# Optimization experiments

Measured on AMD Instinct MI355X. Metric: run time of the kernel, lower is better.

## Reference

```python
import jax, jax.numpy as jnp
import numpy as np

HIDDEN = 1024
N_HEADS = 16
HEAD_DIM = HIDDEN // N_HEADS


def setup_inputs() -> dict:
    key = jax.random.key(0)
    ks = jax.random.split(key, 10)
    s = 0.02
    return {
        "x": jax.random.normal(ks[0], (2, 2048, HIDDEN), dtype=jnp.float32),
        "wq_w": jax.random.normal(ks[1], (HEAD_DIM, HEAD_DIM), dtype=jnp.float32) * s,
        "wq_b": jax.random.normal(ks[2], (HEAD_DIM,), dtype=jnp.float32) * s,
        "wk_w": jax.random.normal(ks[3], (HEAD_DIM, HEAD_DIM), dtype=jnp.float32) * s,
        "wk_b": jax.random.normal(ks[4], (HEAD_DIM,), dtype=jnp.float32) * s,
        "wv_w": jax.random.normal(ks[5], (HEAD_DIM, HEAD_DIM), dtype=jnp.float32) * s,
        "wv_b": jax.random.normal(ks[6], (HEAD_DIM,), dtype=jnp.float32) * s,
        "wo_w": jax.random.normal(ks[7], (HIDDEN, HIDDEN), dtype=jnp.float32) * s,
        "wo_b": jax.random.normal(ks[8], (HIDDEN,), dtype=jnp.float32) * s,
    }


def reference(x, wq_w, wq_b, wk_w, wk_b, wv_w, wv_b, wo_w, wo_b):
    B, S, _ = x.shape
    # Faithful to torch: plain reshape (view), NOT a transpose-based head split.
    xh = x.reshape(B, N_HEADS, S, HEAD_DIM)  # [B,H,S,D]
    # torch Linear: y = x @ W.T + b
    Q = jnp.einsum('bhsd,ed->bhse', xh, wq_w) + wq_b
    K = jnp.einsum('bhsd,ed->bhse', xh, wk_w) + wk_b
    V = jnp.einsum('bhsd,ed->bhse', xh, wv_w) + wv_b
    scale = 1.0 / jnp.sqrt(jnp.float32(HEAD_DIM))
    scores = jnp.einsum('bhqd,bhkd->bhqk', Q, K) * scale  # [B,H,S,S]
    attn = jax.nn.softmax(scores, axis=-1)
    ctx = jnp.einsum('bhqk,bhkd->bhqd', attn, V)  # [B,H,S,D]
    out = ctx.reshape(B, S, HIDDEN)
    return out @ wo_w.T + wo_b
```

## Files before the change

### kernel.cpp

```cpp
#include <hip/hip_runtime.h>
#include <hip/hip_bf16.h>

#define SEQ 2048
#define BHCOUNT 32
#define NROWS (BHCOUNT*SEQ)

typedef unsigned short u16;
typedef unsigned int u32;
using bf16x8 = __attribute__((ext_vector_type(8))) short;
using f32x4  = __attribute__((ext_vector_type(4))) float;

__device__ __forceinline__ float bf2f(u16 h) {
    return __uint_as_float(((u32)h) << 16);
}
__device__ __forceinline__ u16 f2bf(float f) {
    u32 u = __float_as_uint(f);
    u32 r = (u + 0x7FFFu + ((u >> 16) & 1u)) >> 16;
    return (u16)r;
}
__device__ __forceinline__ float fexp2(float x) {
    float r; asm("v_exp_f32 %0, %1" : "=v"(r) : "v"(x)); return r;
}

__device__ __forceinline__ void gload16(const u16* g, u16* l) {
    __builtin_amdgcn_global_load_lds(
        (const __attribute__((address_space(1))) u32*)g,
        (__attribute__((address_space(3))) u32*)l, 16, 0, 0);
}

__device__ __forceinline__ void cvt8(const float* src, float sc, u16* o) {
    float4 a = *(const float4*)src;
    float4 b = *(const float4*)(src + 4);
    o[0]=f2bf(a.x*sc); o[1]=f2bf(a.y*sc); o[2]=f2bf(a.z*sc); o[3]=f2bf(a.w*sc);
    o[4]=f2bf(b.x*sc); o[5]=f2bf(b.y*sc); o[6]=f2bf(b.z*sc); o[7]=f2bf(b.w*sc);
}

__global__ __launch_bounds__(256) void qkv_wconv_kernel(
    const float* __restrict__ x,
    const float* __restrict__ wq, const float* __restrict__ bq,
    const float* __restrict__ wk, const float* __restrict__ bk,
    const float* __restrict__ wv, const float* __restrict__ bv,
    const float* __restrict__ wo,
    u16* __restrict__ Q, u16* __restrict__ K, u16* __restrict__ Vg,
    u16* __restrict__ wob_t)
{
    __shared__ u16 xs[128*64];
    __shared__ u16 ws[192*64];
    __shared__ float bs[192];
    const int t = threadIdx.x;

    if (blockIdx.x >= 512) {
        int g = (blockIdx.x - 512)*256 + t;
        int tile = g >> 9, within = g & 511;
        int row = within >> 3, ks = within & 7;
        int cb = tile >> 4, kt = tile & 15;
        u16 o[8];
        cvt8(&wo[(size_t)(cb*64 + row)*1024 + kt*64 + ks*8], 1.f, o);
        *(uint4*)&wob_t[(size_t)g*8] = *(uint4*)o;
        return;
    }

    const int wid = t >> 6, lane = t & 63;
    const int ln = lane & 15, g4 = lane >> 4;
    const int blk = blockIdx.x;
    const int m0 = blk * 128;
    const int bh = blk >> 4;
    const int ktg0 = (blk & 15) * 2;
    const float qscale = 0.125f * 1.44269504f;

    #pragma unroll
    for (int c = 0; c < 6; ++c) {
        int slot = c*256 + t;
        int row = slot >> 3, ks = slot & 7;
        const float* wsrc = (c < 2) ? wq : (c < 4) ? wk : wv;
        float sc = (c < 2) ? qscale : 1.f;
        u16 o[8];
        cvt8(&wsrc[(row & 63)*64 + ks*8], sc, o);
        *(uint4*)&ws[row*64 + ((ks ^ (row & 7)) << 3)] = *(uint4*)o;
    }
    #pragma unroll
    for (int c = 0; c < 4; ++c) {
        int slot = c*256 + t;
        int row = slot >> 3, ks = slot & 7;
        u16 o[8];
        cvt8(&x[(size_t)(m0 + row)*64 + ks*8], 1.f, o);
        *(uint4*)&xs[row*64 + ((ks ^ (row & 7)) << 3)] = *(uint4*)o;
    }
    if (t < 192) {
        int p = t >> 6, e = t & 63;
        bs[t] = (p == 0) ? bq[e]*qscale : (p == 1) ? bk[e] : bv[e];
    }
    __syncthreads();

    bf16x8 af[2][2];
    #pragma unroll
    for (int mf = 0; mf < 2; ++mf)
        #pragma unroll
        for (int kf = 0; kf < 2; ++kf) {
            int arow = wid*32 + mf*16 + ln;
            af[mf][kf] = *(const bf16x8*)&xs[arow*64 + (((kf*4 + g4) ^ (arow & 7)) << 3)];
        }

    #pragma unroll
    for (int p = 0; p < 2; ++p) {
        bf16x8 bfr[4][2];
        #pragma unroll
        for (int nt = 0; nt < 4; ++nt)
            #pragma unroll
            for (int kf = 0; kf < 2; ++kf) {
                int brow = p*64 + nt*16 + ln;
                bfr[nt][kf] = *(const bf16x8*)&ws[brow*64 + (((kf*4 + g4) ^ (ln & 7)) << 3)];
            }
        f32x4 acc[2][4];
        #pragma unroll
        for (int mf = 0; mf < 2; ++mf)
            #pragma unroll
            for (int nt = 0; nt < 4; ++nt) acc[mf][nt] = (f32x4){0.f,0.f,0.f,0.f};
        #pragma unroll
        for (int kf = 0; kf < 2; ++kf)
            #pragma unroll
            for (int mf = 0; mf < 2; ++mf)
                #pragma unroll
                for (int nt = 0; nt < 4; ++nt)
                    acc[mf][nt] = __builtin_amdgcn_mfma_f32_16x16x32_bf16(
                        af[mf][kf], bfr[nt][kf], acc[mf][nt], 0, 0, 0);
        u16* dst = p ? K : Q;
        #pragma unroll
        for (int mf = 0; mf < 2; ++mf)
            #pragma unroll
            for (int nt = 0; nt < 4; ++nt) {
                float bv4 = bs[p*64 + nt*16 + ln];
                #pragma unroll
                for (int r = 0; r < 4; ++r)
                    dst[(size_t)(m0 + wid*32 + mf*16 + g4*4 + r)*64 + nt*16 + ln]
                        = f2bf(acc[mf][nt][r] + bv4);
            }
    }

    bf16x8 wvf[4][2];
    #pragma unroll
    for (int et = 0; et < 4; ++et)
        #pragma unroll
        for (int kf = 0; kf < 2; ++kf) {
            int brow = 128 + et*16 + ln;
            wvf[et][kf] = *(const bf16x8*)&ws[brow*64 + (((kf*4 + g4) ^ (ln & 7)) << 3)];
        }
    f32x4 vacc[4][2];
    #pragma unroll
    for (int et = 0; et < 4; ++et)
        #pragma unroll
        for (int st = 0; st < 2; ++st) vacc[et][st] = (f32x4){0.f,0.f,0.f,0.f};
    #pragma unroll
    for (int kf = 0; kf < 2; ++kf)
        #pragma unroll
        for (int et = 0; et < 4; ++et)
            #pragma unroll
            for (int st = 0; st < 2; ++st)
                vacc[et][st] = __builtin_amdgcn_mfma_f32_16x16x32_bf16(
                    wvf[et][kf], af[st][kf], vacc[et][st], 0, 0, 0);

    __syncthreads();
    u16* vstage = xs;
    #pragma unroll
    for (int et = 0; et < 4; ++et)
        #pragma unroll
        for (int st = 0; st < 2; ++st)
            #pragma unroll
            for (int r = 0; r < 4; ++r) {
                int e = et*16 + g4*4 + r;
                int s = wid*32 + st*16 + ln;
                vstage[e*128 + ((s + 2*e) & 127)] = f2bf(vacc[et][st][r] + bs[128 + e]);
            }
    __syncthreads();

    #pragma unroll
    for (int c = 0; c < 8; ++c) {
        int j = c*256 + t;
        int kt2 = j >> 10, within = j & 1023;
        int ee = within >> 4, kp0 = (within & 15) * 4;
        int sbase = ((kp0 & 4) << 3) | ((kp0 & 32) >> 1) | ((kp0 & 24) >> 1);
        u16 o[4];
        #pragma unroll
        for (int i = 0; i < 4; ++i)
            o[i] = vstage[ee*128 + ((kt2*64 + sbase + i + 2*ee) & 127)];
        *(uint2*)&Vg[((size_t)bh*32 + ktg0 + kt2)*4096 + ee*64 + kp0] = *(uint2*)o;
    }
}

__device__ __forceinline__ void qkt_tile(
    const u16* Ks, const int (&foff)[4][2], const bf16x8 (&qf)[2], f32x4 (&sacc)[4])
{
    __builtin_amdgcn_s_setprio(1);
    #pragma unroll
    for (int nt = 0; nt < 4; ++nt) {
        sacc[nt] = (f32x4){0.f, 0.f, 0.f, 0.f};
        #pragma unroll
        for (int kf = 0; kf < 2; ++kf)
            sacc[nt] = __builtin_amdgcn_mfma_f32_16x16x32_bf16(
                *(const bf16x8*)&Ks[foff[nt][kf]], qf[kf], sacc[nt], 0, 0, 0);
    }
    __builtin_amdgcn_s_setprio(0);
}

__device__ __forceinline__ void sm_pv(
    f32x4 (&sacc)[4], f32x4 (&oacc)[4], f32x4& lacc,
    const u16* Vts, const int (&foff)[4][2], const bf16x8& ones)
{
    #pragma unroll
    for (int nt = 0; nt < 4; ++nt)
        #pragma unroll
        for (int r = 0; r < 4; ++r)
            sacc[nt][r] = fexp2(sacc[nt][r]);

    union PU { u32 w[4]; bf16x8 v; } pu0, pu1;
    asm("v_cvt_pk_bf16_f32 %0, %1, %2" : "=v"(pu0.w[0]) : "v"(sacc[0][0]), "v"(sacc[0][1]));
    asm("v_cvt_pk_bf16_f32 %0, %1, %2" : "=v"(pu0.w[1]) : "v"(sacc[0][2]), "v"(sacc[0][3]));
    asm("v_cvt_pk_bf16_f32 %0, %1, %2" : "=v"(pu0.w[2]) : "v"(sacc[2][0]), "v"(sacc[2][1]));
    asm("v_cvt_pk_bf16_f32 %0, %1, %2" : "=v"(pu0.w[3]) : "v"(sacc[2][2]), "v"(sacc[2][3]));
    asm("v_cvt_pk_bf16_f32 %0, %1, %2" : "=v"(pu1.w[0]) : "v"(sacc[1][0]), "v"(sacc[1][1]));
    asm("v_cvt_pk_bf16_f32 %0, %1, %2" : "=v"(pu1.w[1]) : "v"(sacc[1][2]), "v"(sacc[1][3]));
    asm("v_cvt_pk_bf16_f32 %0, %1, %2" : "=v"(pu1.w[2]) : "v"(sacc[3][0]), "v"(sacc[3][1]));
    asm("v_cvt_pk_bf16_f32 %0, %1, %2" : "=v"(pu1.w[3]) : "v"(sacc[3][2]), "v"(sacc[3][3]));
    bf16x8 pf[2] = { pu0.v, pu1.v };

    __builtin_amdgcn_s_setprio(1);
    #pragma unroll
    for (int dt = 0; dt < 4; ++dt)
        #pragma unroll
        for (int kf = 0; kf < 2; ++kf)
            oacc[dt] = __builtin_amdgcn_mfma_f32_16x16x32_bf16(
                pf[kf], *(const bf16x8*)&Vts[foff[dt][kf]], oacc[dt], 0, 0, 0);
    #pragma unroll
    for (int kf = 0; kf < 2; ++kf)
        lacc = __builtin_amdgcn_mfma_f32_16x16x32_bf16(pf[kf], ones, lacc, 0, 0, 0);
    __builtin_amdgcn_s_setprio(0);
}

__global__ __launch_bounds__(512) void attn_kernel(
    const u16* __restrict__ Q, const u16* __restrict__ K,
    const u16* __restrict__ Vg, u16* __restrict__ ctx)
{
    __shared__ u16 Kls[3*4096];
    __shared__ u16 Vls[3*4096];

    const int t = threadIdx.x;
    const int wid = t >> 6, lane = t & 63;
    const int ln = lane & 15, g4 = lane >> 4;
    const int bh = blockIdx.y;
    const size_t base   = (size_t)bh * SEQ * 64;
    const size_t vgbase = (size_t)bh * 32 * 4096;
    const int q0 = blockIdx.x * 128 + wid * 16;

    int goff;
    {
        int row = t >> 3, ks = t & 7;
        goff = row*64 + ((ks ^ (row & 7)) << 3);
    }
    const int ldst = wid * 512;

    int foff[4][2];
    #pragma unroll
    for (int nt = 0; nt < 4; ++nt)
        #pragma unroll
        for (int kf = 0; kf < 2; ++kf) {
            int frow = nt*16 + ln;
            foff[nt][kf] = frow*64 + (((kf*4 + g4) ^ (frow & 7)) << 3);
        }

    bf16x8 qf[2];
    #pragma unroll
    for (int kf = 0; kf < 2; ++kf)
        qf[kf] = *(const bf16x8*)&Q[base + (size_t)(q0 + ln)*64 + kf*32 + g4*8];

    bf16x8 ones;
    #pragma unroll
    for (int i = 0; i < 8; ++i) ones[i] = (short)0x3F80;

    f32x4 oacc[4];
    #pragma unroll
    for (int i = 0; i < 4; ++i) oacc[i] = (f32x4){0.f, 0.f, 0.f, 0.f};
    f32x4 lacc = (f32x4){0.f, 0.f, 0.f, 0.f};

    gload16(&K [base   + goff], &Kls[ldst]);
    gload16(&Vg[vgbase + goff], &Vls[ldst]);
    gload16(&K [base   + 4096 + goff], &Kls[4096 + ldst]);
    gload16(&Vg[vgbase + 4096 + goff], &Vls[4096 + ldst]);
    const u16* kptr = &K [base   + 2*4096 + goff];
    const u16* vptr = &Vg[vgbase + 2*4096 + goff];
    __syncthreads();

    f32x4 sA[4], sB[4];
    qkt_tile(&Kls[0], foff, qf, sA);

    #define ABODY(PREV, CUR, SP, SC, SN, STG)                               \
        do {                                                                \
            __syncthreads();                                                \
            if (STG) {                                                      \
                gload16(kptr, &Kls[(SN)*4096 + ldst]);                      \
                gload16(vptr, &Vls[(SN)*4096 + ldst]);                      \
                kptr += 4096; vptr += 4096;                                 \
            }                                                               \
            qkt_tile(&Kls[(SC)*4096], foff, qf, CUR);                       \
            sm_pv(PREV, oacc, lacc, &Vls[(SP)*4096], foff, ones);           \
        } while (0)

    for (int c = 0; c < 5; ++c) {
        ABODY(sA, sB, 0, 1, 2, 1);
        ABODY(sB, sA, 1, 2, 0, 1);
        ABODY(sA, sB, 2, 0, 1, 1);
        ABODY(sB, sA, 0, 1, 2, 1);
        ABODY(sA, sB, 1, 2, 0, 1);
        ABODY(sB, sA, 2, 0, 1, 1);
    }
    ABODY(sA, sB, 0, 1, 2, 0);
    sm_pv(sB, oacc, lacc, &Vls[1*4096], foff, ones);

    #undef ABODY

    #pragma unroll
    for (int r = 0; r < 4; ++r) {
        float inv = 1.f / lacc[r];
        size_t row = base + (size_t)(q0 + g4*4 + r)*64;
        #pragma unroll
        for (int dt = 0; dt < 4; ++dt)
            ctx[row + dt*16 + ln] = f2bf(oacc[dt][r] * inv);
    }
}

__global__ __launch_bounds__(256) void oproj_kernel(
    const u16* __restrict__ ctx, const u16* __restrict__ wob_t,
    const float* __restrict__ bo, float* __restrict__ out)
{
    __shared__ u16 Als[2][128*64];
    __shared__ u16 Bls[2][64*64];
    const int t = threadIdx.x;
    const int wid = t >> 6, lane = t & 63;
    const int ln = lane & 15, g4 = lane >> 4;
    const int wr = wid >> 1, wc = wid & 1;
    const int rb = blockIdx.x, cb = blockIdx.y;
    const int m0 = rb * 128;

    int gA[4], gB[2];
    #pragma unroll
    for (int c = 0; c < 4; ++c) {
        int slot = c*256 + t;
        int row = slot >> 3, ks = slot & 7;
        gA[c] = row*1024 + ((ks ^ (row & 7)) << 3);
    }
    #pragma unroll
    for (int c = 0; c < 2; ++c) {
        int slot = c*256 + t;
        int row = slot >> 3, ks = slot & 7;
        gB[c] = row*64 + ((ks ^ (row & 7)) << 3);
    }
    const u16* actx = ctx + (size_t)m0*1024;
    const u16* bw   = wob_t + (size_t)cb*16*4096;

    f32x4 acc[4][2];
    #pragma unroll
    for (int mf = 0; mf < 4; ++mf)
        #pragma unroll
        for (int nf = 0; nf < 2; ++nf)
            acc[mf][nf] = (f32x4){0.f, 0.f, 0.f, 0.f};

    #pragma unroll
    for (int c = 0; c < 4; ++c) gload16(&actx[gA[c]], &Als[0][(c*256+t)*8]);
    #pragma unroll
    for (int c = 0; c < 2; ++c) gload16(&bw[gB[c]],   &Bls[0][(c*256+t)*8]);
    __syncthreads();

    for (int kt2 = 0; kt2 < 8; ++kt2) {
        #pragma unroll
        for (int half = 0; half < 2; ++half) {
            const int kt = kt2*2 + half;
            if (kt < 15) {
                #pragma unroll
                for (int c = 0; c < 4; ++c)
                    gload16(&actx[(kt+1)*64 + gA[c]], &Als[half^1][(c*256+t)*8]);
                #pragma unroll
                for (int c = 0; c < 2; ++c)
                    gload16(&bw[(kt+1)*4096 + gB[c]], &Bls[half^1][(c*256+t)*8]);
            }
            const u16* As = Als[half];
            const u16* Bs = Bls[half];

            __builtin_amdgcn_s_setprio(1);
            #pragma unroll
            for (int kf = 0; kf < 2; ++kf) {
                bf16x8 af[4], bfr[2];
                #pragma unroll
                for (int mf = 0; mf < 4; ++mf) {
                    int arow = wr*64 + mf*16 + ln;
                    af[mf] = *(const bf16x8*)&As[arow*64 + (((kf*4 + g4) ^ (arow & 7)) << 3)];
                }
                #pragma unroll
                for (int nf = 0; nf < 2; ++nf) {
                    int brow = wc*32 + nf*16 + ln;
                    bfr[nf] = *(const bf16x8*)&Bs[brow*64 + (((kf*4 + g4) ^ (brow & 7)) << 3)];
                }
                #pragma unroll
                for (int mf = 0; mf < 4; ++mf)
                    #pragma unroll
                    for (int nf = 0; nf < 2; ++nf)
                        acc[mf][nf] = __builtin_amdgcn_mfma_f32_16x16x32_bf16(
                            af[mf], bfr[nf], acc[mf][nf], 0, 0, 0);
            }
            __builtin_amdgcn_s_setprio(0);

            __syncthreads();
        }
    }

    #pragma unroll
    for (int mf = 0; mf < 4; ++mf)
        #pragma unroll
        for (int r = 0; r < 4; ++r) {
            int m = m0 + wr*64 + mf*16 + g4*4 + r;
            #pragma unroll
            for (int nf = 0; nf < 2; ++nf) {
                int col = cb*64 + wc*32 + nf*16 + ln;
                out[(size_t)m*1024 + col] = acc[mf][nf][r] + bo[col];
            }
        }
}

extern "C" void kernel_launch(void* const* d_in, const int* in_sizes, int n_in,
                              void* d_out, int out_size, void* d_ws, size_t ws_size,
                              hipStream_t stream) {
    (void)in_sizes; (void)n_in; (void)out_size; (void)ws_size;
    const float* x  = (const float*)d_in[0];
    const float* wq = (const float*)d_in[1];
    const float* bq = (const float*)d_in[2];
    const float* wk = (const float*)d_in[3];
    const float* bk = (const float*)d_in[4];
    const float* wv = (const float*)d_in[5];
    const float* bv = (const float*)d_in[6];
    const float* wo = (const float*)d_in[7];
    const float* bo = (const float*)d_in[8];
    float* out = (float*)d_out;

    u16* Qb  = (u16*)d_ws;
    u16* Kb  = Qb + (size_t)NROWS*64;
    u16* Vgb = Kb + (size_t)NROWS*64;
    u16* ctx = Vgb + (size_t)NROWS*64;
    u16* wob_t = ctx + (size_t)NROWS*64;

    qkv_wconv_kernel<<<dim3(1024), 256, 0, stream>>>(
        x, wq, bq, wk, bk, wv, bv, wo, Qb, Kb, Vgb, wob_t);
    attn_kernel<<<dim3(16, 32), 512, 0, stream>>>(Qb, Kb, Vgb, ctx);
    oproj_kernel<<<dim3(32, 16), 256, 0, stream>>>(ctx, wob_t, bo, out);
}
```

Before: 71.40 us.

## Give each attention wave two query tiles, reusing K/V fragments with double buffering

The attention kernel now launches 256-thread blocks where each wave handles 32 query rows (two 16-row tiles). Each K and V fragment read from LDS feeds two MFMAs, which halves LDS fragment traffic per unit of work. The old triple-buffered, software-pipelined loop that overlapped QK^T of one tile with softmax·V of the previous one is replaced by a simpler double-buffered loop with one barrier per tile. The trade-offs are fewer waves per block, higher register pressure, and the loss of the cross-tile overlap between QK^T and PV.

```diff
diff --git a/kernel.cpp b/kernel.cpp
--- a/kernel.cpp
+++ b/kernel.cpp
@@ -187,61 +187,12 @@
     }
 }
 
-__device__ __forceinline__ void qkt_tile(
-    const u16* Ks, const int (&foff)[4][2], const bf16x8 (&qf)[2], f32x4 (&sacc)[4])
-{
-    __builtin_amdgcn_s_setprio(1);
-    #pragma unroll
-    for (int nt = 0; nt < 4; ++nt) {
-        sacc[nt] = (f32x4){0.f, 0.f, 0.f, 0.f};
-        #pragma unroll
-        for (int kf = 0; kf < 2; ++kf)
-            sacc[nt] = __builtin_amdgcn_mfma_f32_16x16x32_bf16(
-                *(const bf16x8*)&Ks[foff[nt][kf]], qf[kf], sacc[nt], 0, 0, 0);
-    }
-    __builtin_amdgcn_s_setprio(0);
-}
-
-__device__ __forceinline__ void sm_pv(
-    f32x4 (&sacc)[4], f32x4 (&oacc)[4], f32x4& lacc,
-    const u16* Vts, const int (&foff)[4][2], const bf16x8& ones)
-{
-    #pragma unroll
-    for (int nt = 0; nt < 4; ++nt)
-        #pragma unroll
-        for (int r = 0; r < 4; ++r)
-            sacc[nt][r] = fexp2(sacc[nt][r]);
-
-    union PU { u32 w[4]; bf16x8 v; } pu0, pu1;
-    asm("v_cvt_pk_bf16_f32 %0, %1, %2" : "=v"(pu0.w[0]) : "v"(sacc[0][0]), "v"(sacc[0][1]));
-    asm("v_cvt_pk_bf16_f32 %0, %1, %2" : "=v"(pu0.w[1]) : "v"(sacc[0][2]), "v"(sacc[0][3]));
-    asm("v_cvt_pk_bf16_f32 %0, %1, %2" : "=v"(pu0.w[2]) : "v"(sacc[2][0]), "v"(sacc[2][1]));
-    asm("v_cvt_pk_bf16_f32 %0, %1, %2" : "=v"(pu0.w[3]) : "v"(sacc[2][2]), "v"(sacc[2][3]));
-    asm("v_cvt_pk_bf16_f32 %0, %1, %2" : "=v"(pu1.w[0]) : "v"(sacc[1][0]), "v"(sacc[1][1]));
-    asm("v_cvt_pk_bf16_f32 %0, %1, %2" : "=v"(pu1.w[1]) : "v"(sacc[1][2]), "v"(sacc[1][3]));
-    asm("v_cvt_pk_bf16_f32 %0, %1, %2" : "=v"(pu1.w[2]) : "v"(sacc[3][0]), "v"(sacc[3][1]));
-    asm("v_cvt_pk_bf16_f32 %0, %1, %2" : "=v"(pu1.w[3]) : "v"(sacc[3][2]), "v"(sacc[3][3]));
-    bf16x8 pf[2] = { pu0.v, pu1.v };
-
-    __builtin_amdgcn_s_setprio(1);
-    #pragma unroll
-    for (int dt = 0; dt < 4; ++dt)
-        #pragma unroll
-        for (int kf = 0; kf < 2; ++kf)
-            oacc[dt] = __builtin_amdgcn_mfma_f32_16x16x32_bf16(
-                pf[kf], *(const bf16x8*)&Vts[foff[dt][kf]], oacc[dt], 0, 0, 0);
-    #pragma unroll
-    for (int kf = 0; kf < 2; ++kf)
-        lacc = __builtin_amdgcn_mfma_f32_16x16x32_bf16(pf[kf], ones, lacc, 0, 0, 0);
-    __builtin_amdgcn_s_setprio(0);
-}
-
-__global__ __launch_bounds__(512) void attn_kernel(
+__global__ __launch_bounds__(256, 2) void attn_kernel(
     const u16* __restrict__ Q, const u16* __restrict__ K,
     const u16* __restrict__ Vg, u16* __restrict__ ctx)
 {
-    __shared__ u16 Kls[3*4096];
-    __shared__ u16 Vls[3*4096];
+    __shared__ u16 Kls[2][4096];
+    __shared__ u16 Vls[2][4096];
 
     const int t = threadIdx.x;
     const int wid = t >> 6, lane = t & 63;
@@ -249,14 +200,15 @@
     const int bh = blockIdx.y;
     const size_t base   = (size_t)bh * SEQ * 64;
     const size_t vgbase = (size_t)bh * 32 * 4096;
-    const int q0 = blockIdx.x * 128 + wid * 16;
-
-    int goff;
-    {
-        int row = t >> 3, ks = t & 7;
-        goff = row*64 + ((ks ^ (row & 7)) << 3);
-    }
-    const int ldst = wid * 512;
+    const int q0 = blockIdx.x * 128 + wid * 32;
+
+    int goff[2];
+    #pragma unroll
+    for (int c = 0; c < 2; ++c) {
+        int s = c*256 + t;
+        int row = s >> 3, ks = s & 7;
+        goff[c] = row*64 + ((ks ^ (row & 7)) << 3);
+    }
 
     int foff[4][2];
     #pragma unroll
@@ -267,63 +219,125 @@
             foff[nt][kf] = frow*64 + (((kf*4 + g4) ^ (frow & 7)) << 3);
         }
 
-    bf16x8 qf[2];
-    #pragma unroll
-    for (int kf = 0; kf < 2; ++kf)
-        qf[kf] = *(const bf16x8*)&Q[base + (size_t)(q0 + ln)*64 + kf*32 + g4*8];
+    bf16x8 qf0[2], qf1[2];
+    #pragma unroll
+    for (int kf = 0; kf < 2; ++kf) {
+        qf0[kf] = *(const bf16x8*)&Q[base + (size_t)(q0 + ln)*64      + kf*32 + g4*8];
+        qf1[kf] = *(const bf16x8*)&Q[base + (size_t)(q0 + 16 + ln)*64 + kf*32 + g4*8];
+    }
 
     bf16x8 ones;
     #pragma unroll
     for (int i = 0; i < 8; ++i) ones[i] = (short)0x3F80;
 
-    f32x4 oacc[4];
-    #pragma unroll
-    for (int i = 0; i < 4; ++i) oacc[i] = (f32x4){0.f, 0.f, 0.f, 0.f};
-    f32x4 lacc = (f32x4){0.f, 0.f, 0.f, 0.f};
-
-    gload16(&K [base   + goff], &Kls[ldst]);
-    gload16(&Vg[vgbase + goff], &Vls[ldst]);
-    gload16(&K [base   + 4096 + goff], &Kls[4096 + ldst]);
-    gload16(&Vg[vgbase + 4096 + goff], &Vls[4096 + ldst]);
-    const u16* kptr = &K [base   + 2*4096 + goff];
-    const u16* vptr = &Vg[vgbase + 2*4096 + goff];
+    f32x4 oacc0[4], oacc1[4];
+    #pragma unroll
+    for (int i = 0; i < 4; ++i) {
+        oacc0[i] = (f32x4){0.f, 0.f, 0.f, 0.f};
+        oacc1[i] = (f32x4){0.f, 0.f, 0.f, 0.f};
+    }
+    f32x4 lacc0 = (f32x4){0.f, 0.f, 0.f, 0.f};
+    f32x4 lacc1 = (f32x4){0.f, 0.f, 0.f, 0.f};
+
+    #pragma unroll
+    for (int c = 0; c < 2; ++c) {
+        gload16(&K [base   + goff[c]], &Kls[0][c*2048 + wid*512]);
+        gload16(&Vg[vgbase + goff[c]], &Vls[0][c*2048 + wid*512]);
+    }
     __syncthreads();
 
-    f32x4 sA[4], sB[4];
-    qkt_tile(&Kls[0], foff, qf, sA);
-
-    #define ABODY(PREV, CUR, SP, SC, SN, STG)                               \
-        do {                                                                \
-            __syncthreads();                                                \
-            if (STG) {                                                      \
-                gload16(kptr, &Kls[(SN)*4096 + ldst]);                      \
-                gload16(vptr, &Vls[(SN)*4096 + ldst]);                      \
-                kptr += 4096; vptr += 4096;                                 \
-            }                                                               \
-            qkt_tile(&Kls[(SC)*4096], foff, qf, CUR);                       \
-            sm_pv(PREV, oacc, lacc, &Vls[(SP)*4096], foff, ones);           \
-        } while (0)
-
-    for (int c = 0; c < 5; ++c) {
-        ABODY(sA, sB, 0, 1, 2, 1);
-        ABODY(sB, sA, 1, 2, 0, 1);
-        ABODY(sA, sB, 2, 0, 1, 1);
-        ABODY(sB, sA, 0, 1, 2, 1);
-        ABODY(sA, sB, 1, 2, 0, 1);
-        ABODY(sB, sA, 2, 0, 1, 1);
-    }
-    ABODY(sA, sB, 0, 1, 2, 0);
-    sm_pv(sB, oacc, lacc, &Vls[1*4096], foff, ones);
-
-    #undef ABODY
+    for (int kt2 = 0; kt2 < 16; ++kt2) {
+        #pragma unroll
+        for (int half = 0; half < 2; ++half) {
+            const int kt = kt2*2 + half;
+            if (kt < 31) {
+                #pragma unroll
+                for (int c = 0; c < 2; ++c) {
+                    gload16(&K [base   + (size_t)(kt+1)*4096 + goff[c]],
+                            &Kls[half^1][c*2048 + wid*512]);
+                    gload16(&Vg[vgbase + (size_t)(kt+1)*4096 + goff[c]],
+                            &Vls[half^1][c*2048 + wid*512]);
+                }
+            }
+            const u16* Ks  = Kls[half];
+            const u16* Vts = Vls[half];
+
+            f32x4 s0[4], s1[4];
+            #pragma unroll
+            for (int nt = 0; nt < 4; ++nt) {
+                s0[nt] = (f32x4){0.f, 0.f, 0.f, 0.f};
+                s1[nt] = (f32x4){0.f, 0.f, 0.f, 0.f};
+            }
+            __builtin_amdgcn_s_setprio(1);
+            #pragma unroll
+            for (int nt = 0; nt < 4; ++nt)
+                #pragma unroll
+                for (int kf = 0; kf < 2; ++kf) {
+                    bf16x8 kfr = *(const bf16x8*)&Ks[foff[nt][kf]];
+                    s0[nt] = __builtin_amdgcn_mfma_f32_16x16x32_bf16(kfr, qf0[kf], s0[nt], 0, 0, 0);
+                    s1[nt] = __builtin_amdgcn_mfma_f32_16x16x32_bf16(kfr, qf1[kf], s1[nt], 0, 0, 0);
+                }
+            __builtin_amdgcn_s_setprio(0);
+
+            #pragma unroll
+            for (int nt = 0; nt < 4; ++nt)
+                #pragma unroll
+                for (int r = 0; r < 4; ++r) {
+                    s0[nt][r] = fexp2(s0[nt][r]);
+                    s1[nt][r] = fexp2(s1[nt][r]);
+                }
+
+            union PU { u32 w[4]; bf16x8 v; } a0, a1, b0, b1;
+            asm("v_cvt_pk_bf16_f32 %0, %1, %2" : "=v"(a0.w[0]) : "v"(s0[0][0]), "v"(s0[0][1]));
+            asm("v_cvt_pk_bf16_f32 %0, %1, %2" : "=v"(a0.w[1]) : "v"(s0[0][2]), "v"(s0[0][3]));
+            asm("v_cvt_pk_bf16_f32 %0, %1, %2" : "=v"(a0.w[2]) : "v"(s0[2][0]), "v"(s0[2][1]));
+            asm("v_cvt_pk_bf16_f32 %0, %1, %2" : "=v"(a0.w[3]) : "v"(s0[2][2]), "v"(s0[2][3]));
+            asm("v_cvt_pk_bf16_f32 %0, %1, %2" : "=v"(a1.w[0]) : "v"(s0[1][0]), "v"(s0[1][1]));
+            asm("v_cvt_pk_bf16_f32 %0, %1, %2" : "=v"(a1.w[1]) : "v"(s0[1][2]), "v"(s0[1][3]));
+            asm("v_cvt_pk_bf16_f32 %0, %1, %2" : "=v"(a1.w[2]) : "v"(s0[3][0]), "v"(s0[3][1]));
+            asm("v_cvt_pk_bf16_f32 %0, %1, %2" : "=v"(a1.w[3]) : "v"(s0[3][2]), "v"(s0[3][3]));
+            asm("v_cvt_pk_bf16_f32 %0, %1, %2" : "=v"(b0.w[0]) : "v"(s1[0][0]), "v"(s1[0][1]));
+            asm("v_cvt_pk_bf16_f32 %0, %1, %2" : "=v"(b0.w[1]) : "v"(s1[0][2]), "v"(s1[0][3]));
+            asm("v_cvt_pk_bf16_f32 %0, %1, %2" : "=v"(b0.w[2]) : "v"(s1[2][0]), "v"(s1[2][1]));
+            asm("v_cvt_pk_bf16_f32 %0, %1, %2" : "=v"(b0.w[3]) : "v"(s1[2][2]), "v"(s1[2][3]));
+            asm("v_cvt_pk_bf16_f32 %0, %1, %2" : "=v"(b1.w[0]) : "v"(s1[1][0]), "v"(s1[1][1]));
+            asm("v_cvt_pk_bf16_f32 %0, %1, %2" : "=v"(b1.w[1]) : "v"(s1[1][2]), "v"(s1[1][3]));
+            asm("v_cvt_pk_bf16_f32 %0, %1, %2" : "=v"(b1.w[2]) : "v"(s1[3][0]), "v"(s1[3][1]));
+            asm("v_cvt_pk_bf16_f32 %0, %1, %2" : "=v"(b1.w[3]) : "v"(s1[3][2]), "v"(s1[3][3]));
+            bf16x8 pf0[2] = { a0.v, a1.v };
+            bf16x8 pf1[2] = { b0.v, b1.v };
+
+            __builtin_amdgcn_s_setprio(1);
+            #pragma unroll
+            for (int dt = 0; dt < 4; ++dt)
+                #pragma unroll
+                for (int kf = 0; kf < 2; ++kf) {
+                    bf16x8 vfr = *(const bf16x8*)&Vts[foff[dt][kf]];
+                    oacc0[dt] = __builtin_amdgcn_mfma_f32_16x16x32_bf16(pf0[kf], vfr, oacc0[dt], 0, 0, 0);
+                    oacc1[dt] = __builtin_amdgcn_mfma_f32_16x16x32_bf16(pf1[kf], vfr, oacc1[dt], 0, 0, 0);
+                }
+            #pragma unroll
+            for (int kf = 0; kf < 2; ++kf) {
+                lacc0 = __builtin_amdgcn_mfma_f32_16x16x32_bf16(pf0[kf], ones, lacc0, 0, 0, 0);
+                lacc1 = __builtin_amdgcn_mfma_f32_16x16x32_bf16(pf1[kf], ones, lacc1, 0, 0, 0);
+            }
+            __builtin_amdgcn_s_setprio(0);
+
+            __syncthreads();
+        }
+    }
 
     #pragma unroll
     for (int r = 0; r < 4; ++r) {
-        float inv = 1.f / lacc[r];
-        size_t row = base + (size_t)(q0 + g4*4 + r)*64;
-        #pragma unroll
-        for (int dt = 0; dt < 4; ++dt)
-            ctx[row + dt*16 + ln] = f2bf(oacc[dt][r] * inv);
+        float inv0 = 1.f / lacc0[r];
+        float inv1 = 1.f / lacc1[r];
+        size_t row0 = base + (size_t)(q0 + g4*4 + r)*64;
+        size_t row1 = base + (size_t)(q0 + 16 + g4*4 + r)*64;
+        #pragma unroll
+        for (int dt = 0; dt < 4; ++dt) {
+            ctx[row0 + dt*16 + ln] = f2bf(oacc0[dt][r] * inv0);
+            ctx[row1 + dt*16 + ln] = f2bf(oacc1[dt][r] * inv1);
+        }
     }
 }
 
@@ -447,6 +461,6 @@
 
     qkv_wconv_kernel<<<dim3(1024), 256, 0, stream>>>(
         x, wq, bq, wk, bk, wv, bv, wo, Qb, Kb, Vgb, wob_t);
-    attn_kernel<<<dim3(16, 32), 512, 0, stream>>>(Qb, Kb, Vgb, ctx);
+    attn_kernel<<<dim3(16, 32), 256, 0, stream>>>(Qb, Kb, Vgb, ctx);
     oproj_kernel<<<dim3(32, 16), 256, 0, stream>>>(ctx, wob_t, bo, out);
 }
```

Result: no change. 70.76 us (-0.9%).

## Shrink attention blocks to four waves with a simple double-buffered K/V loop

Applied to the files above, without the earlier changes.

The attention kernel moves from 512-thread blocks covering 128 queries to 256-thread blocks covering 64 queries, which doubles the grid and allows up to four blocks per CU. The triple-buffered K/V ring is replaced by a double buffer. The QK^T of the next tile no longer overlaps the softmax/PV of the previous one; each tile now runs QK^T, exp and PV back to back, followed by a barrier. The aim is better latency hiding through occupancy and finer load balancing, at the cost of reading K/V from global memory twice as often and losing the explicit software pipelining.

```diff
diff --git a/kernel.cpp b/kernel.cpp
--- a/kernel.cpp
+++ b/kernel.cpp
@@ -187,61 +187,12 @@
     }
 }
 
-__device__ __forceinline__ void qkt_tile(
-    const u16* Ks, const int (&foff)[4][2], const bf16x8 (&qf)[2], f32x4 (&sacc)[4])
-{
-    __builtin_amdgcn_s_setprio(1);
-    #pragma unroll
-    for (int nt = 0; nt < 4; ++nt) {
-        sacc[nt] = (f32x4){0.f, 0.f, 0.f, 0.f};
-        #pragma unroll
-        for (int kf = 0; kf < 2; ++kf)
-            sacc[nt] = __builtin_amdgcn_mfma_f32_16x16x32_bf16(
-                *(const bf16x8*)&Ks[foff[nt][kf]], qf[kf], sacc[nt], 0, 0, 0);
-    }
-    __builtin_amdgcn_s_setprio(0);
-}
-
-__device__ __forceinline__ void sm_pv(
-    f32x4 (&sacc)[4], f32x4 (&oacc)[4], f32x4& lacc,
-    const u16* Vts, const int (&foff)[4][2], const bf16x8& ones)
-{
-    #pragma unroll
-    for (int nt = 0; nt < 4; ++nt)
-        #pragma unroll
-        for (int r = 0; r < 4; ++r)
-            sacc[nt][r] = fexp2(sacc[nt][r]);
-
-    union PU { u32 w[4]; bf16x8 v; } pu0, pu1;
-    asm("v_cvt_pk_bf16_f32 %0, %1, %2" : "=v"(pu0.w[0]) : "v"(sacc[0][0]), "v"(sacc[0][1]));
-    asm("v_cvt_pk_bf16_f32 %0, %1, %2" : "=v"(pu0.w[1]) : "v"(sacc[0][2]), "v"(sacc[0][3]));
-    asm("v_cvt_pk_bf16_f32 %0, %1, %2" : "=v"(pu0.w[2]) : "v"(sacc[2][0]), "v"(sacc[2][1]));
-    asm("v_cvt_pk_bf16_f32 %0, %1, %2" : "=v"(pu0.w[3]) : "v"(sacc[2][2]), "v"(sacc[2][3]));
-    asm("v_cvt_pk_bf16_f32 %0, %1, %2" : "=v"(pu1.w[0]) : "v"(sacc[1][0]), "v"(sacc[1][1]));
-    asm("v_cvt_pk_bf16_f32 %0, %1, %2" : "=v"(pu1.w[1]) : "v"(sacc[1][2]), "v"(sacc[1][3]));
-    asm("v_cvt_pk_bf16_f32 %0, %1, %2" : "=v"(pu1.w[2]) : "v"(sacc[3][0]), "v"(sacc[3][1]));
-    asm("v_cvt_pk_bf16_f32 %0, %1, %2" : "=v"(pu1.w[3]) : "v"(sacc[3][2]), "v"(sacc[3][3]));
-    bf16x8 pf[2] = { pu0.v, pu1.v };
-
-    __builtin_amdgcn_s_setprio(1);
-    #pragma unroll
-    for (int dt = 0; dt < 4; ++dt)
-        #pragma unroll
-        for (int kf = 0; kf < 2; ++kf)
-            oacc[dt] = __builtin_amdgcn_mfma_f32_16x16x32_bf16(
-                pf[kf], *(const bf16x8*)&Vts[foff[dt][kf]], oacc[dt], 0, 0, 0);
-    #pragma unroll
-    for (int kf = 0; kf < 2; ++kf)
-        lacc = __builtin_amdgcn_mfma_f32_16x16x32_bf16(pf[kf], ones, lacc, 0, 0, 0);
-    __builtin_amdgcn_s_setprio(0);
-}
-
-__global__ __launch_bounds__(512) void attn_kernel(
+__global__ __launch_bounds__(256, 4) void attn_kernel(
     const u16* __restrict__ Q, const u16* __restrict__ K,
     const u16* __restrict__ Vg, u16* __restrict__ ctx)
 {
-    __shared__ u16 Kls[3*4096];
-    __shared__ u16 Vls[3*4096];
+    __shared__ u16 Kls[2][4096];
+    __shared__ u16 Vls[2][4096];
 
     const int t = threadIdx.x;
     const int wid = t >> 6, lane = t & 63;
@@ -249,14 +200,15 @@
     const int bh = blockIdx.y;
     const size_t base   = (size_t)bh * SEQ * 64;
     const size_t vgbase = (size_t)bh * 32 * 4096;
-    const int q0 = blockIdx.x * 128 + wid * 16;
-
-    int goff;
-    {
-        int row = t >> 3, ks = t & 7;
-        goff = row*64 + ((ks ^ (row & 7)) << 3);
-    }
-    const int ldst = wid * 512;
+    const int q0 = blockIdx.x * 64 + wid * 16;
+
+    int goff[2];
+    #pragma unroll
+    for (int c = 0; c < 2; ++c) {
+        int s = c*256 + t;
+        int row = s >> 3, ks = s & 7;
+        goff[c] = row*64 + ((ks ^ (row & 7)) << 3);
+    }
 
     int foff[4][2];
     #pragma unroll
@@ -281,41 +233,73 @@
     for (int i = 0; i < 4; ++i) oacc[i] = (f32x4){0.f, 0.f, 0.f, 0.f};
     f32x4 lacc = (f32x4){0.f, 0.f, 0.f, 0.f};
 
-    gload16(&K [base   + goff], &Kls[ldst]);
-    gload16(&Vg[vgbase + goff], &Vls[ldst]);
-    gload16(&K [base   + 4096 + goff], &Kls[4096 + ldst]);
-    gload16(&Vg[vgbase + 4096 + goff], &Vls[4096 + ldst]);
-    const u16* kptr = &K [base   + 2*4096 + goff];
-    const u16* vptr = &Vg[vgbase + 2*4096 + goff];
+    #pragma unroll
+    for (int c = 0; c < 2; ++c) {
+        gload16(&K [base   + goff[c]], &Kls[0][c*2048 + wid*512]);
+        gload16(&Vg[vgbase + goff[c]], &Vls[0][c*2048 + wid*512]);
+    }
     __syncthreads();
 
-    f32x4 sA[4], sB[4];
-    qkt_tile(&Kls[0], foff, qf, sA);
-
-    #define ABODY(PREV, CUR, SP, SC, SN, STG)                               \
-        do {                                                                \
-            __syncthreads();                                                \
-            if (STG) {                                                      \
-                gload16(kptr, &Kls[(SN)*4096 + ldst]);                      \
-                gload16(vptr, &Vls[(SN)*4096 + ldst]);                      \
-                kptr += 4096; vptr += 4096;                                 \
-            }                                                               \
-            qkt_tile(&Kls[(SC)*4096], foff, qf, CUR);                       \
-            sm_pv(PREV, oacc, lacc, &Vls[(SP)*4096], foff, ones);           \
-        } while (0)
-
-    for (int c = 0; c < 5; ++c) {
-        ABODY(sA, sB, 0, 1, 2, 1);
-        ABODY(sB, sA, 1, 2, 0, 1);
-        ABODY(sA, sB, 2, 0, 1, 1);
-        ABODY(sB, sA, 0, 1, 2, 1);
-        ABODY(sA, sB, 1, 2, 0, 1);
-        ABODY(sB, sA, 2, 0, 1, 1);
-    }
-    ABODY(sA, sB, 0, 1, 2, 0);
-    sm_pv(sB, oacc, lacc, &Vls[1*4096], foff, ones);
-
-    #undef ABODY
+    for (int kt2 = 0; kt2 < 16; ++kt2) {
+        #pragma unroll
+        for (int half = 0; half < 2; ++half) {
+            const int kt = kt2*2 + half;
+            if (kt < 31) {
+                #pragma unroll
+                for (int c = 0; c < 2; ++c) {
+                    gload16(&K [base   + (size_t)(kt+1)*4096 + goff[c]],
+                            &Kls[half^1][c*2048 + wid*512]);
+                    gload16(&Vg[vgbase + (size_t)(kt+1)*4096 + goff[c]],
+                            &Vls[half^1][c*2048 + wid*512]);
+                }
+            }
+            const u16* Ks  = Kls[half];
+            const u16* Vts = Vls[half];
+
+            f32x4 sacc[4];
+            #pragma unroll
+            for (int nt = 0; nt < 4; ++nt) sacc[nt] = (f32x4){0.f, 0.f, 0.f, 0.f};
+            __builtin_amdgcn_s_setprio(1);
+            #pragma unroll
+            for (int nt = 0; nt < 4; ++nt)
+                #pragma unroll
+                for (int kf = 0; kf < 2; ++kf)
+                    sacc[nt] = __builtin_amdgcn_mfma_f32_16x16x32_bf16(
+                        *(const bf16x8*)&Ks[foff[nt][kf]], qf[kf], sacc[nt], 0, 0, 0);
+            __builtin_amdgcn_s_setprio(0);
+
+            #pragma unroll
+            for (int nt = 0; nt < 4; ++nt)
+                #pragma unroll
+                for (int r = 0; r < 4; ++r)
+                    sacc[nt][r] = fexp2(sacc[nt][r]);
+
+            union PU { u32 w[4]; bf16x8 v; } pu0, pu1;
+            asm("v_cvt_pk_bf16_f32 %0, %1, %2" : "=v"(pu0.w[0]) : "v"(sacc[0][0]), "v"(sacc[0][1]));
+            asm("v_cvt_pk_bf16_f32 %0, %1, %2" : "=v"(pu0.w[1]) : "v"(sacc[0][2]), "v"(sacc[0][3]));
+            asm("v_cvt_pk_bf16_f32 %0, %1, %2" : "=v"(pu0.w[2]) : "v"(sacc[2][0]), "v"(sacc[2][1]));
+            asm("v_cvt_pk_bf16_f32 %0, %1, %2" : "=v"(pu0.w[3]) : "v"(sacc[2][2]), "v"(sacc[2][3]));
+            asm("v_cvt_pk_bf16_f32 %0, %1, %2" : "=v"(pu1.w[0]) : "v"(sacc[1][0]), "v"(sacc[1][1]));
+            asm("v_cvt_pk_bf16_f32 %0, %1, %2" : "=v"(pu1.w[1]) : "v"(sacc[1][2]), "v"(sacc[1][3]));
+            asm("v_cvt_pk_bf16_f32 %0, %1, %2" : "=v"(pu1.w[2]) : "v"(sacc[3][0]), "v"(sacc[3][1]));
+            asm("v_cvt_pk_bf16_f32 %0, %1, %2" : "=v"(pu1.w[3]) : "v"(sacc[3][2]), "v"(sacc[3][3]));
+            bf16x8 pf[2] = { pu0.v, pu1.v };
+
+            __builtin_amdgcn_s_setprio(1);
+            #pragma unroll
+            for (int dt = 0; dt < 4; ++dt)
+                #pragma unroll
+                for (int kf = 0; kf < 2; ++kf)
+                    oacc[dt] = __builtin_amdgcn_mfma_f32_16x16x32_bf16(
+                        pf[kf], *(const bf16x8*)&Vts[foff[dt][kf]], oacc[dt], 0, 0, 0);
+            #pragma unroll
+            for (int kf = 0; kf < 2; ++kf)
+                lacc = __builtin_amdgcn_mfma_f32_16x16x32_bf16(pf[kf], ones, lacc, 0, 0, 0);
+            __builtin_amdgcn_s_setprio(0);
+
+            __syncthreads();
+        }
+    }
 
     #pragma unroll
     for (int r = 0; r < 4; ++r) {
@@ -447,6 +431,6 @@
 
     qkv_wconv_kernel<<<dim3(1024), 256, 0, stream>>>(
         x, wq, bq, wk, bk, wv, bv, wo, Qb, Kb, Vgb, wob_t);
-    attn_kernel<<<dim3(16, 32), 512, 0, stream>>>(Qb, Kb, Vgb, ctx);
+    attn_kernel<<<dim3(32, 32), 256, 0, stream>>>(Qb, Kb, Vgb, ctx);
     oproj_kernel<<<dim3(32, 16), 256, 0, stream>>>(ctx, wob_t, bo, out);
 }
```

After: 76.54 us. +7.2%, slower.
